# Optimization experiments

Measured on AMD Instinct MI355X. Metric: run time of the kernel, lower is better.

The kernel has to match this reference:

```python
import jax, jax.numpy as jnp
import numpy as np
import math

B, L, D = 4, 4096, 1024
H = 16
DH = D // H  # 64
MAX_SEQ = 8192
NF_MAX = MAX_SEQ // 2 + 1  # 4097
EPS = 1e-6
SQRT2_INV = 1.0 / math.sqrt(2.0)


def _ln(x, scale, bias, eps=1e-5):
    m = jnp.mean(x, axis=-1, keepdims=True)
    v = jnp.mean((x - m) ** 2, axis=-1, keepdims=True)
    return (x - m) * jax.lax.rsqrt(v + eps) * scale + bias


def setup_inputs() -> dict:
    key = jax.random.key(0)
    ks = jax.random.split(key, 16)
    s = 0.02
    inp = {
        'x': jax.random.normal(ks[0], (B, L, D), dtype=jnp.float32),
        'Wq': jax.random.normal(ks[1], (D, D), dtype=jnp.float32) * s,
        'Wv': jax.random.normal(ks[2], (D, D), dtype=jnp.float32) * s,
        'Wo': jax.random.normal(ks[3], (D, D), dtype=jnp.float32) * s,
        # gate MLP: LayerNorm(Dh) -> Linear(Dh,4Dh) -> GELU -> Linear(4Dh, 2*NF_MAX)
        'ln_g_s': jnp.ones((DH,), jnp.float32),
        'ln_g_b': jnp.zeros((DH,), jnp.float32),
        'W1': jax.random.normal(ks[4], (4 * DH, DH), dtype=jnp.float32) * s,
        'b1': jnp.zeros((4 * DH,), jnp.float32),
        'W2': jax.random.normal(ks[5], (2 * NF_MAX, 4 * DH), dtype=jnp.float32) * s,
        'b2': jnp.zeros((2 * NF_MAX,), jnp.float32),
        'modrelu_bias': jnp.zeros((H, NF_MAX), jnp.float32),
        # wavelet gating MLP on head_dim
        'ln_w_s': jnp.ones((DH,), jnp.float32),
        'ln_w_b': jnp.zeros((DH,), jnp.float32),
        'Ww1': jax.random.normal(ks[6], (DH, DH), dtype=jnp.float32) * s,
        'bw1': jnp.zeros((DH,), jnp.float32),
        'Ww2': jax.random.normal(ks[7], (DH, DH), dtype=jnp.float32) * s,
        'bw2': jnp.zeros((DH,), jnp.float32),
    }
    return inp


def _spectre_forward(x, Wq, Wv, Wo, ln_g_s, ln_g_b, W1, b1, W2, b2,
                     modrelu_bias, ln_w_s, ln_w_b, Ww1, bw1, Ww2, bw2):
    b, l, d = x.shape
    n_freq = l // 2 + 1
    # projections -> (B,H,L,Dh)
    q = jnp.einsum('bld,ed->ble', x, Wq).reshape(b, l, H, DH).transpose(0, 2, 1, 3)
    v = jnp.einsum('bld,ed->ble', x, Wv).reshape(b, l, H, DH).transpose(0, 2, 1, 3)
    q_bar = jnp.mean(q, axis=2)  # (B,H,Dh) global query
    # frequency gates from global query
    h = _ln(q_bar, ln_g_s, ln_g_b)
    h = jax.nn.gelu(jnp.einsum('bhd,fd->bhf', h, W1) + b1, approximate=False)
    g = jnp.einsum('bhf,gf->bhg', h, W2) + b2  # (B,H,2*NF_MAX)
    gate = g[..., :n_freq] + 1j * g[..., NF_MAX:NF_MAX + n_freq]  # (B,H,n_freq)
    # spectral mixing along sequence axis
    Vf = jnp.fft.rfft(v, axis=2)  # (B,H,n_freq,Dh) complex
    Vf = Vf * gate[..., None]
    # modReLU nonlinearity on complex spectrum
    mag = jnp.abs(Vf)
    bias = modrelu_bias[None, :, :n_freq, None]
    Vf = Vf * (jax.nn.relu(mag + bias) / (mag + EPS))
    y = jnp.fft.irfft(Vf, n=l, axis=2)  # (B,H,L,Dh)
    # wavelet refinement (eval mode -> never skipped)
    gw = _ln(q_bar, ln_w_s, ln_w_b)
    gw = jax.nn.gelu(jnp.einsum('bhd,ed->bhe', gw, Ww1) + bw1, approximate=False)
    gw = jax.nn.sigmoid(jnp.einsum('bhd,ed->bhe', gw, Ww2) + bw2)  # (B,H,Dh)
    yc = y.transpose(0, 1, 3, 2)  # (B,H,Dh,L)
    low = (yc[..., 0::2] + yc[..., 1::2]) * SQRT2_INV   # Haar analysis LP
    high = (yc[..., 1::2] - yc[..., 0::2]) * SQRT2_INV  # Haar analysis HP
    low = low * gw[..., None]
    high = high * gw[..., None]
    even = (low - high) * SQRT2_INV   # Haar synthesis
    odd = (low + high) * SQRT2_INV
    rec = jnp.stack([even, odd], axis=-1).reshape(b, H, DH, l)  # interleave
    y = y + rec.transpose(0, 1, 3, 2)
    out = jnp.einsum('bld,ed->ble', y.transpose(0, 2, 1, 3).reshape(b, l, d), Wo)
    return out


def reference(x, Wq, Wv, Wo, ln_g_s, ln_g_b, W1, b1, W2, b2,
              modrelu_bias, ln_w_s, ln_w_b, Ww1, bw1, Ww2, bw2):
    return _spectre_forward(x, Wq, Wv, Wo, ln_g_s, ln_g_b, W1, b1, W2, b2,
                            modrelu_bias, ln_w_s, ln_w_b, Ww1, bw1, Ww2, bw2)
```

## Files before the change

### kernel.cpp

```cpp
#include <hip/hip_runtime.h>
#include <math.h>

#define LSEQ 4096
#define DDIM 1024
#define NB 4
#define NH 16
#define DHD 64
#define NFREQ 2049
#define NFMAX 4097

typedef __bf16 bf16_8 __attribute__((ext_vector_type(8)));
typedef float f32x4 __attribute__((ext_vector_type(4)));
typedef float f2 __attribute__((ext_vector_type(2)));

__device__ __forceinline__ float gelu_exact(float v) {
    return 0.5f * v * (1.0f + erff(v * 0.70710678118654752440f));
}

__device__ __forceinline__ void gload16(const void* g, void* l) {
    __builtin_amdgcn_global_load_lds((const __attribute__((address_space(1))) char*)g,
                                     (__attribute__((address_space(3))) char*)l, 16, 0, 0);
}

__global__ __launch_bounds__(256) void k_xbar_partial(const float* __restrict__ x, float* __restrict__ xbp,
                                                      __bf16* __restrict__ xbf) {
    int d = blockIdx.x * 256 + threadIdx.x;
    int chunk = blockIdx.y;
    int b = blockIdx.z;
    size_t base = ((size_t)b * LSEQ + (size_t)chunk * 256) * DDIM + d;
    float acc = 0.f;
    for (int l = 0; l < 256; ++l) {
        float v = x[base + (size_t)l * DDIM];
        acc += v;
        xbf[base + (size_t)l * DDIM] = (__bf16)v;
    }
    xbp[(size_t)(b * 16 + chunk) * DDIM + d] = acc;
}

__global__ __launch_bounds__(256) void k_xbar_reduce(const float* __restrict__ xbp, float* __restrict__ xbar) {
    int d = blockIdx.x * 256 + threadIdx.x;
    int b = blockIdx.y;
    float acc = 0.f;
    for (int c = 0; c < 16; ++c) acc += xbp[(size_t)(b * 16 + c) * DDIM + d];
    xbar[b * DDIM + d] = acc * (1.0f / LSEQ);
}

__global__ __launch_bounds__(256) void k_cvt(const float* __restrict__ s, __bf16* __restrict__ d, int n) {
    int i = (blockIdx.x * 256 + threadIdx.x) * 4;
    if (i < n) {
        float4 v = *(const float4*)(s + i);
        d[i] = (__bf16)v.x; d[i + 1] = (__bf16)v.y; d[i + 2] = (__bf16)v.z; d[i + 3] = (__bf16)v.w;
    }
}

__global__ __launch_bounds__(256) void k_qbar(const float* __restrict__ xbar, const float* __restrict__ Wq,
                                              float* __restrict__ qbar) {
    int lane = threadIdx.x & 63;
    int e = blockIdx.x * 4 + (threadIdx.x >> 6);
    const float* wrow = Wq + (size_t)e * DDIM;
    float a0 = 0, a1 = 0, a2 = 0, a3 = 0;
    for (int i = 0; i < 16; ++i) {
        int d = lane + i * 64;
        float w = wrow[d];
        a0 += w * xbar[d];
        a1 += w * xbar[DDIM + d];
        a2 += w * xbar[2 * DDIM + d];
        a3 += w * xbar[3 * DDIM + d];
    }
    for (int off = 32; off > 0; off >>= 1) {
        a0 += __shfl_down(a0, off);
        a1 += __shfl_down(a1, off);
        a2 += __shfl_down(a2, off);
        a3 += __shfl_down(a3, off);
    }
    if (lane == 0) {
        qbar[e] = a0;
        qbar[DDIM + e] = a1;
        qbar[2 * DDIM + e] = a2;
        qbar[3 * DDIM + e] = a3;
    }
}

__global__ __launch_bounds__(256) void k_mlp(const float* __restrict__ qbar,
                                             const float* __restrict__ ln_g_s, const float* __restrict__ ln_g_b,
                                             const float* __restrict__ W1, const float* __restrict__ b1,
                                             const float* __restrict__ ln_w_s, const float* __restrict__ ln_w_b,
                                             const float* __restrict__ Ww1, const float* __restrict__ bw1,
                                             const float* __restrict__ Ww2, const float* __restrict__ bw2,
                                             float* __restrict__ h1g, float* __restrict__ gwp1) {
    int bh = blockIdx.x;
    __shared__ float q[64], hg[64], hw[64], g1[64];
    __shared__ float sm, sv;
    int t = threadIdx.x;
    if (t < 64) q[t] = qbar[bh * 64 + t];
    __syncthreads();
    if (t == 0) {
        float m = 0;
        for (int i = 0; i < 64; ++i) m += q[i];
        m *= (1.0f / 64.0f);
        float v = 0;
        for (int i = 0; i < 64; ++i) { float dd = q[i] - m; v += dd * dd; }
        v *= (1.0f / 64.0f);
        sm = m; sv = v;
    }
    __syncthreads();
    if (t < 64) {
        float n = (q[t] - sm) * rsqrtf(sv + 1e-5f);
        hg[t] = n * ln_g_s[t] + ln_g_b[t];
        hw[t] = n * ln_w_s[t] + ln_w_b[t];
    }
    __syncthreads();
    {
        int f = t;
        const float* w = W1 + (size_t)f * 64;
        float s = b1[f];
        for (int d0 = 0; d0 < 64; ++d0) s += hg[d0] * w[d0];
        h1g[(size_t)bh * 256 + f] = gelu_exact(s);
    }
    if (t < 64) {
        const float* w = Ww1 + (size_t)t * 64;
        float s = bw1[t];
        for (int k = 0; k < 64; ++k) s += hw[k] * w[k];
        g1[t] = gelu_exact(s);
    }
    __syncthreads();
    if (t < 64) {
        const float* w = Ww2 + (size_t)t * 64;
        float s = bw2[t];
        for (int k = 0; k < 64; ++k) s += g1[k] * w[k];
        gwp1[bh * 64 + t] = 1.0f + 1.0f / (1.0f + expf(-s));
    }
}

__global__ __launch_bounds__(256) void k_gate(const float* __restrict__ h1g, const float* __restrict__ W2,
                                              const float* __restrict__ b2,
                                              float* __restrict__ gre, float* __restrict__ gim) {
    int task = blockIdx.x * 4 + (threadIdx.x >> 6);
    if (task >= 2 * NFREQ) return;
    int lane = threadIdx.x & 63;
    int part = task >= NFREQ;
    int f = task - part * NFREQ;
    int row = part ? (NFMAX + f) : f;
    const float* w = W2 + (size_t)row * 256;
    float w0 = w[lane], w1 = w[64 + lane], w2 = w[128 + lane], w3 = w[192 + lane];
    float bias = b2[row];
    float* dst = part ? gim : gre;
    for (int bh = 0; bh < 64; ++bh) {
        const float* hr = h1g + (size_t)bh * 256;
        float p = w0 * hr[lane] + w1 * hr[64 + lane] + w2 * hr[128 + lane] + w3 * hr[192 + lane];
        for (int off = 32; off > 0; off >>= 1) p += __shfl_down(p, off);
        if (lane == 0) dst[(size_t)bh * NFREQ + f] = p + bias;
    }
}

__device__ __forceinline__ void swz256(int bid, int& n0, int& m0, int& b) {
    int w = (bid & 7) * 32 + (bid >> 3);
    b = w >> 6;
    m0 = ((w >> 2) & 15) << 8;
    n0 = (w & 3) << 8;
}

__device__ __forceinline__ void g4_stage(const __bf16* __restrict__ src, int row0, int kt,
                                         char* buf, int tid) {
#pragma unroll
    for (int j = 0; j < 2; ++j) {
        int c = j * 512 + tid;
        int q = c >> 3, p = c & 7;
        int s3 = p ^ (q & 7);
        int r = 2 * q + (s3 >> 2);
        int kc = (s3 & 3) * 8;
        char* dst = buf + (size_t)(j * 512 + (tid & ~63)) * 16;
        gload16(src + ((size_t)(row0 + r) << 10) + kt * 32 + kc, dst);
    }
}

__device__ __forceinline__ void g4_compute(const char* L, int bi, int wm, int wn,
                                           int lane, f32x4 (&acc)[8][4]) {
    int lrow = lane & 15, lsl = lane >> 4;
    const char* Ab = L + bi * 16384;
    const char* Bb = L + 65536 + bi * 16384;
    int s3 = (lrow & 1) * 4 + lsl;
    bf16_8 af[8], bfr[4];
#pragma unroll
    for (int mi = 0; mi < 8; ++mi) {
        int q = wm * 64 + mi * 8 + (lrow >> 1);
        af[mi] = *(const bf16_8*)(Ab + q * 128 + ((s3 ^ (q & 7)) << 4));
    }
#pragma unroll
    for (int ni = 0; ni < 4; ++ni) {
        int q = wn * 32 + ni * 8 + (lrow >> 1);
        bfr[ni] = *(const bf16_8*)(Bb + q * 128 + ((s3 ^ (q & 7)) << 4));
    }
    __builtin_amdgcn_s_setprio(1);
#pragma unroll
    for (int mi = 0; mi < 8; ++mi)
#pragma unroll
        for (int ni = 0; ni < 4; ++ni)
            acc[mi][ni] = __builtin_amdgcn_mfma_f32_16x16x32_bf16(af[mi], bfr[ni], acc[mi][ni], 0, 0, 0);
    __builtin_amdgcn_s_setprio(0);
}

__device__ __forceinline__ void g4_core(const __bf16* __restrict__ A, const __bf16* __restrict__ B,
                                        int m0, int n0, char* L, f32x4 (&acc)[8][4]) {
    int tid = threadIdx.x;
    int lane = tid & 63, w = tid >> 6;
    int wm = w >> 2, wn = w & 3;
#pragma unroll
    for (int mi = 0; mi < 8; ++mi)
#pragma unroll
        for (int ni = 0; ni < 4; ++ni) acc[mi][ni] = (f32x4){0.f, 0.f, 0.f, 0.f};

#define G4_STAGE(KT, BI)                                   \
    do {                                                   \
        g4_stage(A, m0, (KT), L + (BI) * 16384, tid);      \
        g4_stage(B, n0, (KT), L + 65536 + (BI) * 16384, tid); \
    } while (0)

    G4_STAGE(0, 0);
    G4_STAGE(1, 1);
    G4_STAGE(2, 2);
    asm volatile("s_waitcnt vmcnt(8)" ::: "memory");
    __builtin_amdgcn_s_barrier();
    asm volatile("" ::: "memory");
#pragma unroll 1
    for (int kt = 0; kt < 32; ++kt) {
        int bi = kt & 3;
        if (kt < 29) {
            G4_STAGE(kt + 3, (kt + 3) & 3);
        }
        g4_compute(L, bi, wm, wn, lane, acc);
        asm volatile("s_waitcnt lgkmcnt(0)" ::: "memory");
        if (kt <= 28) {
            asm volatile("s_waitcnt vmcnt(8)" ::: "memory");
        } else if (kt == 29) {
            asm volatile("s_waitcnt vmcnt(4)" ::: "memory");
        } else if (kt == 30) {
            asm volatile("s_waitcnt vmcnt(0)" ::: "memory");
        }
        __builtin_amdgcn_s_barrier();
        asm volatile("" ::: "memory");
    }
#undef G4_STAGE
}

__global__ __launch_bounds__(512, 2) void k_vgemm(const __bf16* __restrict__ xbf, const __bf16* __restrict__ Wvb,
                                                  __bf16* __restrict__ vt) {
    __shared__ __align__(16) char L[131072 + 17408];
    __bf16 (*st)[16][68] = (__bf16(*)[16][68])(L + 131072);
    int n0, m0, b;
    swz256(blockIdx.x, n0, m0, b);
    f32x4 acc[8][4];
    g4_core(xbf + ((size_t)b << 22), Wvb, m0, n0, L, acc);
    int tid = threadIdx.x;
    int lane = tid & 63, w = tid >> 6;
    int wm = w >> 2, wn = w & 3;
    size_t vbase = ((size_t)b << 22);
#pragma unroll
    for (int ni = 0; ni < 4; ++ni) {
#pragma unroll
        for (int half = 0; half < 2; ++half) {
#pragma unroll
            for (int ml = 0; ml < 4; ++ml)
#pragma unroll
                for (int r = 0; r < 4; ++r)
                    st[w][lane & 15][ml * 16 + (lane >> 4) * 4 + r] = (__bf16)acc[half * 4 + ml][ni][r];
            asm volatile("" ::: "memory");
#pragma unroll
            for (int er = 0; er < 16; ++er) {
                vt[vbase + (size_t)(n0 + wn * 64 + ni * 16 + er) * LSEQ + m0 + wm * 128 + half * 64 + lane] =
                    st[w][er][lane];
            }
            asm volatile("" ::: "memory");
        }
    }
}

__global__ __launch_bounds__(512, 2) void k_ogemm(const __bf16* __restrict__ ybf, const __bf16* __restrict__ Wob,
                                                  float* __restrict__ out) {
    __shared__ __align__(16) char L[131072];
    int n0, m0, b;
    swz256(blockIdx.x, n0, m0, b);
    f32x4 acc[8][4];
    g4_core(ybf + ((size_t)b << 22), Wob, m0, n0, L, acc);
    int tid = threadIdx.x;
    int lane = tid & 63, w = tid >> 6;
    int wm = w >> 2, wn = w & 3;
    float* ob = out + ((size_t)b << 22);
#pragma unroll
    for (int mi = 0; mi < 8; ++mi)
#pragma unroll
        for (int ni = 0; ni < 4; ++ni)
#pragma unroll
            for (int r = 0; r < 4; ++r)
                ob[(size_t)(m0 + wm * 128 + mi * 16 + (lane >> 4) * 4 + r) * DDIM +
                   n0 + wn * 64 + ni * 16 + (lane & 15)] = acc[mi][ni][r];
}

__device__ __forceinline__ f2 cmul2(f2 a, f2 b) {
    f2 t = a * (f2){b.x, b.x};
    f2 ayx = __builtin_shufflevector(a, a, 1, 0);
    return t + ayx * (f2){-b.y, b.y};
}
__device__ __forceinline__ f2 mulmi(f2 v) {
    f2 s = __builtin_shufflevector(v, v, 1, 0);
    return s * (f2){1.f, -1.f};
}
__device__ __forceinline__ f2 mulpi(f2 v) {
    f2 s = __builtin_shufflevector(v, v, 1, 0);
    return s * (f2){-1.f, 1.f};
}
__device__ __forceinline__ int P8(int i) { return i + (i >> 3) + (i >> 8); }
__device__ __forceinline__ int SR8(int k) {
    return ((k & 7) << 8) | (((k >> 3) & 7) << 5) | (((k >> 6) & 7) << 2) | (k >> 9);
}

template <int S>
__device__ __forceinline__ void dft4v(f2* x) {
    f2 t0 = x[0] + x[2], t1 = x[0] - x[2];
    f2 t2 = x[1] + x[3], t3 = x[1] - x[3];
    f2 j3 = (S == 1) ? mulmi(t3) : mulpi(t3);
    x[0] = t0 + t2;
    x[2] = t0 - t2;
    x[1] = t1 + j3;
    x[3] = t1 - j3;
}

template <int S>
__device__ __forceinline__ void dft8v(f2* x) {
    f2 e[4] = {x[0], x[2], x[4], x[6]};
    f2 o[4] = {x[1], x[3], x[5], x[7]};
    dft4v<S>(e);
    dft4v<S>(o);
    const float c = 0.7071067811865476f;
    const float sg = (S == 1) ? -1.f : 1.f;
    o[1] = cmul2(o[1], (f2){c, sg * c});
    o[2] = (S == 1) ? mulmi(o[2]) : mulpi(o[2]);
    o[3] = cmul2(o[3], (f2){-c, sg * c});
    x[0] = e[0] + o[0];
    x[4] = e[0] - o[0];
    x[1] = e[1] + o[1];
    x[5] = e[1] - o[1];
    x[2] = e[2] + o[2];
    x[6] = e[2] - o[2];
    x[3] = e[3] + o[3];
    x[7] = e[3] - o[3];
}

template <int S>
__device__ __forceinline__ void tw8(f2* x, int j, float invN) {
    float base = ((S == 1) ? -6.283185307179586f : 6.283185307179586f) * invN;
    float sn, cs;
    __sincosf(base * (float)j, &sn, &cs);
    f2 w1 = (f2){cs, sn};
    f2 w2 = cmul2(w1, w1);
    f2 w3 = cmul2(w2, w1);
    f2 w4 = cmul2(w2, w2);
    f2 w5 = cmul2(w4, w1);
    f2 w6 = cmul2(w4, w2);
    f2 w7 = cmul2(w4, w3);
    x[1] = cmul2(x[1], w1);
    x[2] = cmul2(x[2], w2);
    x[3] = cmul2(x[3], w3);
    x[4] = cmul2(x[4], w4);
    x[5] = cmul2(x[5], w5);
    x[6] = cmul2(x[6], w6);
    x[7] = cmul2(x[7], w7);
}

__global__ __launch_bounds__(256, 2) void k_fft(__bf16* __restrict__ vty,
                                                const float* __restrict__ gre, const float* __restrict__ gim,
                                                const float* __restrict__ mrb, const float* __restrict__ gwp1) {
    __shared__ f2 Zp[2312];
    int pid = blockIdx.x;
    int b = pid >> 10, e = pid & 1023;
    int h = e >> 6, dh = e & 63;
    int bh = b * 16 + h;
    size_t gbase = (size_t)bh * NFREQ;
    size_t mbase = (size_t)h * NFMAX;
    __bf16* row = vty + ((size_t)b << 22) + ((size_t)e << 12);
    int t = threadIdx.x;

#pragma unroll
    for (int cc = 0; cc < 2; ++cc) {
        int c = t + cc * 256;
        bf16_8 a = *(const bf16_8*)&row[c * 8];
#pragma unroll
        for (int q = 0; q < 4; ++q)
            Zp[P8(c * 4 + q)] = (f2){(float)a[2 * q], (float)a[2 * q + 1]};
    }
    __syncthreads();

    f2 x[8];
    {
#pragma unroll
        for (int r = 0; r < 8; ++r) x[r] = Zp[P8(r * 256 + t)];
        dft8v<1>(x);
        tw8<1>(x, t, 1.0f / 2048.0f);
#pragma unroll
        for (int r = 0; r < 8; ++r) Zp[P8(r * 256 + t)] = x[r];
    }
    __syncthreads();
    {
        int g = t >> 5, j = t & 31, base = g * 256 + j;
#pragma unroll
        for (int r = 0; r < 8; ++r) x[r] = Zp[P8(base + r * 32)];
        dft8v<1>(x);
        tw8<1>(x, j, 1.0f / 256.0f);
#pragma unroll
        for (int r = 0; r < 8; ++r) Zp[P8(base + r * 32)] = x[r];
    }
    __syncthreads();
    {
        int g = t >> 2, j = t & 3, base = g * 32 + j;
#pragma unroll
        for (int r = 0; r < 8; ++r) x[r] = Zp[P8(base + r * 4)];
        dft8v<1>(x);
        tw8<1>(x, j, 1.0f / 32.0f);
#pragma unroll
        for (int r = 0; r < 8; ++r) Zp[P8(base + r * 4)] = x[r];
    }
    __syncthreads();
    {
        int base = t * 8;
#pragma unroll
        for (int q = 0; q < 4; ++q) { x[q] = Zp[P8(base + q)]; x[4 + q] = Zp[P8(base + 4 + q)]; }
        dft4v<1>(x);
        dft4v<1>(x + 4);
#pragma unroll
        for (int q = 0; q < 4; ++q) { Zp[P8(base + q)] = x[q]; Zp[P8(base + 4 + q)] = x[4 + q]; }
    }
    __syncthreads();

    {
        float sn0, cs0;
        __sincosf(-1.5339807878856412e-3f * (float)(1 + t), &sn0, &cs0);
        f2 wk = (f2){cs0, sn0};
        const f2 W256 = (f2){0.92387953251128675613f, -0.38268343236508977172f};
#pragma unroll
        for (int r = 0; r < 4; ++r) {
            int k = 1 + (r << 8) + t;
            int k2 = 2048 - k;
            int sA = P8(SR8(k)), sB = P8(SR8(k2));
            float cs = wk.x, sn = wk.y;
            f2 Za = Zp[sA], Zb = Zp[sB];
            float Er = 0.5f * (Za.x + Zb.x), Ei = 0.5f * (Za.y - Zb.y);
            float Dr = 0.5f * (Za.x - Zb.x), Di = 0.5f * (Za.y + Zb.y);
            float WDr = cs * Dr - sn * Di, WDi = cs * Di + sn * Dr;
            float Tr = -WDi, Ti = WDr;
            float Vkr = Er - Tr, Vki = Ei - Ti;
            float Vk2r = Er + Tr, Vk2i = -(Ei + Ti);
            float g1r = gre[gbase + k], g1i = gim[gbase + k], b1v = mrb[mbase + k];
            float Ykr = Vkr * g1r - Vki * g1i, Yki = Vkr * g1i + Vki * g1r;
            float m1 = sqrtf(Ykr * Ykr + Yki * Yki);
            float s1 = fmaxf(m1 + b1v, 0.f) / (m1 + 1e-6f);
            Ykr *= s1; Yki *= s1;
            float g2r = gre[gbase + k2], g2i = gim[gbase + k2], b2v = mrb[mbase + k2];
            float Yk2r = Vk2r * g2r - Vk2i * g2i, Yk2i = Vk2r * g2i + Vk2i * g2r;
            float m2 = sqrtf(Yk2r * Yk2r + Yk2i * Yk2i);
            float s2 = fmaxf(m2 + b2v, 0.f) / (m2 + 1e-6f);
            Yk2r *= s2; Yk2i *= s2;
            float Epr = 0.5f * (Ykr + Yk2r), Epi = 0.5f * (Yki - Yk2i);
            float Fr = 0.5f * (Ykr - Yk2r), Fi = 0.5f * (Yki + Yk2i);
            float CWFr = cs * Fr + sn * Fi;
            float CWFi = cs * Fi - sn * Fr;
            Zp[sA] = (f2){Epr - CWFi, Epi + CWFr};
            Zp[sB] = (f2){Epr + CWFi, -Epi + CWFr};
            wk = cmul2(wk, W256);
        }
    }
    if (t == 0) {
        f2 Z0 = Zp[P8(0)];
        float V0 = Z0.x + Z0.y, VN = Z0.x - Z0.y;
        float g0r = gre[gbase], g0i = gim[gbase], b0v = mrb[mbase];
        float y0r = V0 * g0r, y0i = V0 * g0i;
        float m0 = sqrtf(y0r * y0r + y0i * y0i);
        float Y0 = y0r * (fmaxf(m0 + b0v, 0.f) / (m0 + 1e-6f));
        float gNr = gre[gbase + 2048], gNi = gim[gbase + 2048], bNv = mrb[mbase + 2048];
        float yNr = VN * gNr, yNi = VN * gNi;
        float mN = sqrtf(yNr * yNr + yNi * yNi);
        float YN = yNr * (fmaxf(mN + bNv, 0.f) / (mN + 1e-6f));
        Zp[P8(0)] = (f2){0.5f * (Y0 + YN), 0.5f * (Y0 - YN)};
    }
    __syncthreads();

    {
        int base = t * 8;
#pragma unroll
        for (int q = 0; q < 4; ++q) { x[q] = Zp[P8(base + q)]; x[4 + q] = Zp[P8(base + 4 + q)]; }
        dft4v<-1>(x);
        dft4v<-1>(x + 4);
#pragma unroll
        for (int q = 0; q < 4; ++q) { Zp[P8(base + q)] = x[q]; Zp[P8(base + 4 + q)] = x[4 + q]; }
    }
    __syncthreads();
    {
        int g = t >> 2, j = t & 3, base = g * 32 + j;
#pragma unroll
        for (int r = 0; r < 8; ++r) x[r] = Zp[P8(base + r * 4)];
        tw8<-1>(x, j, 1.0f / 32.0f);
        dft8v<-1>(x);
#pragma unroll
        for (int r = 0; r < 8; ++r) Zp[P8(base + r * 4)] = x[r];
    }
    __syncthreads();
    {
        int g = t >> 5, j = t & 31, base = g * 256 + j;
#pragma unroll
        for (int r = 0; r < 8; ++r) x[r] = Zp[P8(base + r * 32)];
        tw8<-1>(x, j, 1.0f / 256.0f);
        dft8v<-1>(x);
#pragma unroll
        for (int r = 0; r < 8; ++r) Zp[P8(base + r * 32)] = x[r];
    }
    __syncthreads();
    {
#pragma unroll
        for (int r = 0; r < 8; ++r) x[r] = Zp[P8(r * 256 + t)];
        tw8<-1>(x, t, 1.0f / 2048.0f);
        dft8v<-1>(x);
        float sc = gwp1[bh * 64 + dh] * (1.0f / 2048.0f);
        unsigned int* row32 = (unsigned int*)row;
#pragma unroll
        for (int r = 0; r < 8; ++r) {
            __bf16 h1 = (__bf16)(x[r].x * sc);
            __bf16 h2 = (__bf16)(x[r].y * sc);
            unsigned int u = (unsigned int)__builtin_bit_cast(unsigned short, h1) |
                             ((unsigned int)__builtin_bit_cast(unsigned short, h2) << 16);
            row32[t + 256 * r] = u;
        }
    }
}

__global__ __launch_bounds__(256) void k_t2(const __bf16* __restrict__ vt, __bf16* __restrict__ ybf) {
    __shared__ __bf16 tl[64][66];
    int e0 = blockIdx.x * 64, l0 = blockIdx.y * 64, b = blockIdx.z;
    int t = threadIdx.x;
    const __bf16* src = vt + ((size_t)b << 22);
    __bf16* dst = ybf + ((size_t)b << 22);
    int er = t >> 3, lc = (t & 7) * 8;
#pragma unroll
    for (int it = 0; it < 2; ++it) {
        int e = er + it * 32;
        bf16_8 v = *(const bf16_8*)&src[(size_t)(e0 + e) * LSEQ + l0 + lc];
#pragma unroll
        for (int j = 0; j < 8; ++j) tl[e][lc + j] = v[j];
    }
    __syncthreads();
    int lr = t >> 3, ec = (t & 7) * 8;
#pragma unroll
    for (int it = 0; it < 2; ++it) {
        int l = lr + it * 32;
        bf16_8 v;
#pragma unroll
        for (int j = 0; j < 8; ++j) v[j] = tl[ec + j][l];
        *(bf16_8*)&dst[(size_t)(l0 + l) * DDIM + e0 + ec] = v;
    }
}

extern "C" void kernel_launch(void* const* d_in, const int* in_sizes, int n_in,
                              void* d_out, int out_size, void* d_ws, size_t ws_size,
                              hipStream_t stream) {
    const float* x      = (const float*)d_in[0];
    const float* Wq     = (const float*)d_in[1];
    const float* Wv     = (const float*)d_in[2];
    const float* Wo     = (const float*)d_in[3];
    const float* ln_g_s = (const float*)d_in[4];
    const float* ln_g_b = (const float*)d_in[5];
    const float* W1     = (const float*)d_in[6];
    const float* b1     = (const float*)d_in[7];
    const float* W2     = (const float*)d_in[8];
    const float* b2     = (const float*)d_in[9];
    const float* mrb    = (const float*)d_in[10];
    const float* ln_w_s = (const float*)d_in[11];
    const float* ln_w_b = (const float*)d_in[12];
    const float* Ww1    = (const float*)d_in[13];
    const float* bw1    = (const float*)d_in[14];
    const float* Ww2    = (const float*)d_in[15];
    const float* bw2    = (const float*)d_in[16];
    float* out = (float*)d_out;

    char* W = (char*)d_ws;
    __bf16* xbf = (__bf16*)W;
    __bf16* ybf = xbf;
    __bf16* Wvb = (__bf16*)(W + 33554432);
    __bf16* Wob = (__bf16*)(W + 35651584);
    float*  xbp = (float*)(W + 37748736);
    float*  xbar= (float*)(W + 38010880);
    float*  qbar= (float*)(W + 38027264);
    float*  h1g = (float*)(W + 38043648);
    float*  gwp1= (float*)(W + 38109184);
    float*  gre = (float*)(W + 38125568);
    float*  gim = (float*)(W + 38650112);

    __bf16* vt = (__bf16*)d_out;

    k_xbar_partial<<<dim3(4, 16, 4), 256, 0, stream>>>(x, xbp, xbf);
    k_cvt<<<1024, 256, 0, stream>>>(Wv, Wvb, DDIM * DDIM);
    k_cvt<<<1024, 256, 0, stream>>>(Wo, Wob, DDIM * DDIM);
    k_xbar_reduce<<<dim3(4, 4), 256, 0, stream>>>(xbp, xbar);
    k_qbar<<<256, 256, 0, stream>>>(xbar, Wq, qbar);
    k_mlp<<<64, 256, 0, stream>>>(qbar, ln_g_s, ln_g_b, W1, b1, ln_w_s, ln_w_b,
                                  Ww1, bw1, Ww2, bw2, h1g, gwp1);
    k_gate<<<1025, 256, 0, stream>>>(h1g, W2, b2, gre, gim);
    k_vgemm<<<256, 512, 0, stream>>>(xbf, Wvb, vt);
    k_fft<<<4096, 256, 0, stream>>>(vt, gre, gim, mrb, gwp1);
    k_t2<<<dim3(16, 64, 4), 256, 0, stream>>>(vt, ybf);
    k_ogemm<<<256, 512, 0, stream>>>(ybf, Wob, out);
}
```

Before: 194.3 us.

## Shrink GEMM tiles to 128x256 with 3-stage LDS ring for more blocks

The V-projection and output-projection GEMMs now use 128x256 tiles instead of 256x256, which doubles the grid to 512 blocks. The shared-memory ring drops from 4 stages to 3 and LDS use falls from about 144KB to 72KB. Launch bounds rise to allow 4 blocks per CU, and the block swizzle is updated for the new tile count. The aim is to fill all CUs on the MI355X and gain occupancy, at the cost of lower arithmetic intensity per tile, more redundant loads of the B operand, and a shallower prefetch pipeline.

```diff
diff --git a/kernel.cpp b/kernel.cpp
--- a/kernel.cpp
+++ b/kernel.cpp
@@ -153,17 +153,18 @@
     }
 }
 
-__device__ __forceinline__ void swz256(int bid, int& n0, int& m0, int& b) {
-    int w = (bid & 7) * 32 + (bid >> 3);
-    b = w >> 6;
-    m0 = ((w >> 2) & 15) << 8;
+__device__ __forceinline__ void swz512(int bid, int& n0, int& m0, int& b) {
+    int w = (bid & 7) * 64 + (bid >> 3);
+    b = w >> 7;
+    m0 = ((w >> 2) & 31) << 7;
     n0 = (w & 3) << 8;
 }
 
-__device__ __forceinline__ void g4_stage(const __bf16* __restrict__ src, int row0, int kt,
+template <int NCH>
+__device__ __forceinline__ void g5_stage(const __bf16* __restrict__ src, int row0, int kt,
                                          char* buf, int tid) {
 #pragma unroll
-    for (int j = 0; j < 2; ++j) {
+    for (int j = 0; j < NCH; ++j) {
         int c = j * 512 + tid;
         int q = c >> 3, p = c & 7;
         int s3 = p ^ (q & 7);
@@ -174,16 +175,16 @@
     }
 }
 
-__device__ __forceinline__ void g4_compute(const char* L, int bi, int wm, int wn,
-                                           int lane, f32x4 (&acc)[8][4]) {
+__device__ __forceinline__ void g5_compute(const char* L, int bi, int wm, int wn,
+                                           int lane, f32x4 (&acc)[4][4]) {
     int lrow = lane & 15, lsl = lane >> 4;
-    const char* Ab = L + bi * 16384;
-    const char* Bb = L + 65536 + bi * 16384;
+    const char* Ab = L + bi * 8192;
+    const char* Bb = L + 24576 + bi * 16384;
     int s3 = (lrow & 1) * 4 + lsl;
-    bf16_8 af[8], bfr[4];
-#pragma unroll
-    for (int mi = 0; mi < 8; ++mi) {
-        int q = wm * 64 + mi * 8 + (lrow >> 1);
+    bf16_8 af[4], bfr[4];
+#pragma unroll
+    for (int mi = 0; mi < 4; ++mi) {
+        int q = wm * 32 + mi * 8 + (lrow >> 1);
         af[mi] = *(const bf16_8*)(Ab + q * 128 + ((s3 ^ (q & 7)) << 4));
     }
 #pragma unroll
@@ -193,64 +194,60 @@
     }
     __builtin_amdgcn_s_setprio(1);
 #pragma unroll
-    for (int mi = 0; mi < 8; ++mi)
+    for (int mi = 0; mi < 4; ++mi)
 #pragma unroll
         for (int ni = 0; ni < 4; ++ni)
             acc[mi][ni] = __builtin_amdgcn_mfma_f32_16x16x32_bf16(af[mi], bfr[ni], acc[mi][ni], 0, 0, 0);
     __builtin_amdgcn_s_setprio(0);
 }
 
-__device__ __forceinline__ void g4_core(const __bf16* __restrict__ A, const __bf16* __restrict__ B,
-                                        int m0, int n0, char* L, f32x4 (&acc)[8][4]) {
+__device__ __forceinline__ void g5_core(const __bf16* __restrict__ A, const __bf16* __restrict__ B,
+                                        int m0, int n0, char* L, f32x4 (&acc)[4][4]) {
     int tid = threadIdx.x;
     int lane = tid & 63, w = tid >> 6;
     int wm = w >> 2, wn = w & 3;
 #pragma unroll
-    for (int mi = 0; mi < 8; ++mi)
+    for (int mi = 0; mi < 4; ++mi)
 #pragma unroll
         for (int ni = 0; ni < 4; ++ni) acc[mi][ni] = (f32x4){0.f, 0.f, 0.f, 0.f};
 
-#define G4_STAGE(KT, BI)                                   \
-    do {                                                   \
-        g4_stage(A, m0, (KT), L + (BI) * 16384, tid);      \
-        g4_stage(B, n0, (KT), L + 65536 + (BI) * 16384, tid); \
+#define G5_STAGE(KT, BI)                                        \
+    do {                                                        \
+        g5_stage<1>(A, m0, (KT), L + (BI) * 8192, tid);         \
+        g5_stage<2>(B, n0, (KT), L + 24576 + (BI) * 16384, tid);\
     } while (0)
 
-    G4_STAGE(0, 0);
-    G4_STAGE(1, 1);
-    G4_STAGE(2, 2);
-    asm volatile("s_waitcnt vmcnt(8)" ::: "memory");
+    G5_STAGE(0, 0);
+    G5_STAGE(1, 1);
+    asm volatile("s_waitcnt vmcnt(3)" ::: "memory");
     __builtin_amdgcn_s_barrier();
     asm volatile("" ::: "memory");
 #pragma unroll 1
     for (int kt = 0; kt < 32; ++kt) {
-        int bi = kt & 3;
-        if (kt < 29) {
-            G4_STAGE(kt + 3, (kt + 3) & 3);
+        if (kt < 30) {
+            G5_STAGE(kt + 2, (kt + 2) % 3);
         }
-        g4_compute(L, bi, wm, wn, lane, acc);
+        g5_compute(L, kt % 3, wm, wn, lane, acc);
         asm volatile("s_waitcnt lgkmcnt(0)" ::: "memory");
-        if (kt <= 28) {
-            asm volatile("s_waitcnt vmcnt(8)" ::: "memory");
-        } else if (kt == 29) {
-            asm volatile("s_waitcnt vmcnt(4)" ::: "memory");
+        if (kt < 30) {
+            asm volatile("s_waitcnt vmcnt(3)" ::: "memory");
         } else if (kt == 30) {
             asm volatile("s_waitcnt vmcnt(0)" ::: "memory");
         }
         __builtin_amdgcn_s_barrier();
         asm volatile("" ::: "memory");
     }
-#undef G4_STAGE
-}
-
-__global__ __launch_bounds__(512, 2) void k_vgemm(const __bf16* __restrict__ xbf, const __bf16* __restrict__ Wvb,
+#undef G5_STAGE
+}
+
+__global__ __launch_bounds__(512, 4) void k_vgemm(const __bf16* __restrict__ xbf, const __bf16* __restrict__ Wvb,
                                                   __bf16* __restrict__ vt) {
-    __shared__ __align__(16) char L[131072 + 17408];
-    __bf16 (*st)[16][68] = (__bf16(*)[16][68])(L + 131072);
+    __shared__ __align__(16) char L[73728];
     int n0, m0, b;
-    swz256(blockIdx.x, n0, m0, b);
-    f32x4 acc[8][4];
-    g4_core(xbf + ((size_t)b << 22), Wvb, m0, n0, L, acc);
+    swz512(blockIdx.x, n0, m0, b);
+    f32x4 acc[4][4];
+    g5_core(xbf + ((size_t)b << 22), Wvb, m0, n0, L, acc);
+    __bf16 (*st)[16][68] = (__bf16(*)[16][68])L;
     int tid = threadIdx.x;
     int lane = tid & 63, w = tid >> 6;
     int wm = w >> 2, wn = w & 3;
@@ -258,41 +255,38 @@
 #pragma unroll
     for (int ni = 0; ni < 4; ++ni) {
 #pragma unroll
-        for (int half = 0; half < 2; ++half) {
-#pragma unroll
-            for (int ml = 0; ml < 4; ++ml)
-#pragma unroll
-                for (int r = 0; r < 4; ++r)
-                    st[w][lane & 15][ml * 16 + (lane >> 4) * 4 + r] = (__bf16)acc[half * 4 + ml][ni][r];
-            asm volatile("" ::: "memory");
-#pragma unroll
-            for (int er = 0; er < 16; ++er) {
-                vt[vbase + (size_t)(n0 + wn * 64 + ni * 16 + er) * LSEQ + m0 + wm * 128 + half * 64 + lane] =
-                    st[w][er][lane];
-            }
-            asm volatile("" ::: "memory");
+        for (int ml = 0; ml < 4; ++ml)
+#pragma unroll
+            for (int r = 0; r < 4; ++r)
+                st[w][lane & 15][ml * 16 + (lane >> 4) * 4 + r] = (__bf16)acc[ml][ni][r];
+        asm volatile("" ::: "memory");
+#pragma unroll
+        for (int er = 0; er < 16; ++er) {
+            vt[vbase + (size_t)(n0 + wn * 64 + ni * 16 + er) * LSEQ + m0 + wm * 64 + lane] =
+                st[w][er][lane];
         }
-    }
-}
-
-__global__ __launch_bounds__(512, 2) void k_ogemm(const __bf16* __restrict__ ybf, const __bf16* __restrict__ Wob,
+        asm volatile("" ::: "memory");
+    }
+}
+
+__global__ __launch_bounds__(512, 4) void k_ogemm(const __bf16* __restrict__ ybf, const __bf16* __restrict__ Wob,
                                                   float* __restrict__ out) {
-    __shared__ __align__(16) char L[131072];
+    __shared__ __align__(16) char L[73728];
     int n0, m0, b;
-    swz256(blockIdx.x, n0, m0, b);
-    f32x4 acc[8][4];
-    g4_core(ybf + ((size_t)b << 22), Wob, m0, n0, L, acc);
+    swz512(blockIdx.x, n0, m0, b);
+    f32x4 acc[4][4];
+    g5_core(ybf + ((size_t)b << 22), Wob, m0, n0, L, acc);
     int tid = threadIdx.x;
     int lane = tid & 63, w = tid >> 6;
     int wm = w >> 2, wn = w & 3;
     float* ob = out + ((size_t)b << 22);
 #pragma unroll
-    for (int mi = 0; mi < 8; ++mi)
+    for (int mi = 0; mi < 4; ++mi)
 #pragma unroll
         for (int ni = 0; ni < 4; ++ni)
 #pragma unroll
             for (int r = 0; r < 4; ++r)
-                ob[(size_t)(m0 + wm * 128 + mi * 16 + (lane >> 4) * 4 + r) * DDIM +
+                ob[(size_t)(m0 + wm * 64 + mi * 16 + (lane >> 4) * 4 + r) * DDIM +
                    n0 + wn * 64 + ni * 16 + (lane & 15)] = acc[mi][ni][r];
 }
 
@@ -602,8 +596,8 @@
     k_mlp<<<64, 256, 0, stream>>>(qbar, ln_g_s, ln_g_b, W1, b1, ln_w_s, ln_w_b,
                                   Ww1, bw1, Ww2, bw2, h1g, gwp1);
     k_gate<<<1025, 256, 0, stream>>>(h1g, W2, b2, gre, gim);
-    k_vgemm<<<256, 512, 0, stream>>>(xbf, Wvb, vt);
+    k_vgemm<<<512, 512, 0, stream>>>(xbf, Wvb, vt);
     k_fft<<<4096, 256, 0, stream>>>(vt, gre, gim, mrb, gwp1);
     k_t2<<<dim3(16, 64, 4), 256, 0, stream>>>(vt, ybf);
-    k_ogemm<<<256, 512, 0, stream>>>(ybf, Wob, out);
-}
+    k_ogemm<<<512, 512, 0, stream>>>(ybf, Wob, out);
+}
```

Measured after the change: 197.6 us. Within noise of the previous version (+1.7%).

## Restructure bf16 GEMM mainloop into double-buffered 64-wide K stages with interleaved loads

Applied to the files above, without the earlier changes.

Replaces the 4-slot, 32-wide K pipeline in the shared V- and output-projection GEMM core with a 2-slot, 64-wide K double buffer. Each iteration is split into four phases that interleave LDS fragment reads, MFMA batches and async global-to-LDS loads for the next stage. The aim is to hide LDS reads behind MFMA work and overlap global loads with compute, so the core runs at higher MFMA throughput. In exchange it adds many more barriers per iteration and a shallower prefetch depth, which could expose global-load latency.

```diff
diff --git a/kernel.cpp b/kernel.cpp
--- a/kernel.cpp
+++ b/kernel.cpp
@@ -160,7 +160,7 @@
     n0 = (w & 3) << 8;
 }
 
-__device__ __forceinline__ void g4_stage(const __bf16* __restrict__ src, int row0, int kt,
+__device__ __forceinline__ void g6_stage(const __bf16* __restrict__ src, int row0, int kcol0,
                                          char* buf, int tid) {
 #pragma unroll
     for (int j = 0; j < 2; ++j) {
@@ -170,77 +170,106 @@
         int r = 2 * q + (s3 >> 2);
         int kc = (s3 & 3) * 8;
         char* dst = buf + (size_t)(j * 512 + (tid & ~63)) * 16;
-        gload16(src + ((size_t)(row0 + r) << 10) + kt * 32 + kc, dst);
-    }
-}
-
-__device__ __forceinline__ void g4_compute(const char* L, int bi, int wm, int wn,
-                                           int lane, f32x4 (&acc)[8][4]) {
-    int lrow = lane & 15, lsl = lane >> 4;
-    const char* Ab = L + bi * 16384;
-    const char* Bb = L + 65536 + bi * 16384;
-    int s3 = (lrow & 1) * 4 + lsl;
-    bf16_8 af[8], bfr[4];
-#pragma unroll
-    for (int mi = 0; mi < 8; ++mi) {
-        int q = wm * 64 + mi * 8 + (lrow >> 1);
-        af[mi] = *(const bf16_8*)(Ab + q * 128 + ((s3 ^ (q & 7)) << 4));
-    }
-#pragma unroll
-    for (int ni = 0; ni < 4; ++ni) {
-        int q = wn * 32 + ni * 8 + (lrow >> 1);
-        bfr[ni] = *(const bf16_8*)(Bb + q * 128 + ((s3 ^ (q & 7)) << 4));
-    }
+        gload16(src + ((size_t)(row0 + r) << 10) + kcol0 + kc, dst);
+    }
+}
+
+__device__ __forceinline__ void g6_readA(const char* Ah, int wm, int lrow, int lsl, int mi0, bf16_8* af) {
+#pragma unroll
+    for (int i = 0; i < 4; ++i) {
+        int r = wm * 128 + (mi0 + i) * 16 + lrow;
+        int q = r >> 1;
+        int s3 = (r & 1) * 4 + lsl;
+        af[i] = *(const bf16_8*)(Ah + q * 128 + ((s3 ^ (q & 7)) << 4));
+    }
+}
+
+__device__ __forceinline__ void g6_readB(const char* Bh, int wn, int lrow, int lsl, bf16_8* bfr) {
+#pragma unroll
+    for (int i = 0; i < 4; ++i) {
+        int r = wn * 64 + i * 16 + lrow;
+        int q = r >> 1;
+        int s3 = (r & 1) * 4 + lsl;
+        bfr[i] = *(const bf16_8*)(Bh + q * 128 + ((s3 ^ (q & 7)) << 4));
+    }
+}
+
+__device__ __forceinline__ void g6_mfma16(const bf16_8* af, const bf16_8* bfr, int mi0, f32x4 (&acc)[8][4]) {
     __builtin_amdgcn_s_setprio(1);
 #pragma unroll
-    for (int mi = 0; mi < 8; ++mi)
-#pragma unroll
-        for (int ni = 0; ni < 4; ++ni)
-            acc[mi][ni] = __builtin_amdgcn_mfma_f32_16x16x32_bf16(af[mi], bfr[ni], acc[mi][ni], 0, 0, 0);
+    for (int i = 0; i < 4; ++i)
+#pragma unroll
+        for (int j = 0; j < 4; ++j)
+            acc[mi0 + i][j] = __builtin_amdgcn_mfma_f32_16x16x32_bf16(af[i], bfr[j], acc[mi0 + i][j], 0, 0, 0);
     __builtin_amdgcn_s_setprio(0);
 }
 
-__device__ __forceinline__ void g4_core(const __bf16* __restrict__ A, const __bf16* __restrict__ B,
+#define BAR()  do { __builtin_amdgcn_s_barrier(); asm volatile("" ::: "memory"); } while (0)
+#define LGKM0() asm volatile("s_waitcnt lgkmcnt(0)" ::: "memory")
+#define VM(n)   asm volatile("s_waitcnt vmcnt(" #n ")" ::: "memory")
+
+__device__ __forceinline__ void g6_core(const __bf16* __restrict__ A, const __bf16* __restrict__ B,
                                         int m0, int n0, char* L, f32x4 (&acc)[8][4]) {
     int tid = threadIdx.x;
     int lane = tid & 63, w = tid >> 6;
     int wm = w >> 2, wn = w & 3;
+    int lrow = lane & 15, lsl = lane >> 4;
 #pragma unroll
     for (int mi = 0; mi < 8; ++mi)
 #pragma unroll
         for (int ni = 0; ni < 4; ++ni) acc[mi][ni] = (f32x4){0.f, 0.f, 0.f, 0.f};
 
-#define G4_STAGE(KT, BI)                                   \
-    do {                                                   \
-        g4_stage(A, m0, (KT), L + (BI) * 16384, tid);      \
-        g4_stage(B, n0, (KT), L + 65536 + (BI) * 16384, tid); \
-    } while (0)
-
-    G4_STAGE(0, 0);
-    G4_STAGE(1, 1);
-    G4_STAGE(2, 2);
-    asm volatile("s_waitcnt vmcnt(8)" ::: "memory");
-    __builtin_amdgcn_s_barrier();
-    asm volatile("" ::: "memory");
+#define AS(s, h) (L + (s) * 32768 + (h) * 16384)
+#define BS(s, h) (L + 65536 + (s) * 32768 + (h) * 16384)
+
+    g6_stage(A, m0, 0, AS(0, 0), tid);
+    g6_stage(B, n0, 0, BS(0, 0), tid);
+    g6_stage(A, m0, 32, AS(0, 1), tid);
+    g6_stage(B, n0, 32, BS(0, 1), tid);
+    VM(4);
+    BAR();
+
 #pragma unroll 1
-    for (int kt = 0; kt < 32; ++kt) {
-        int bi = kt & 3;
-        if (kt < 29) {
-            G4_STAGE(kt + 3, (kt + 3) & 3);
-        }
-        g4_compute(L, bi, wm, wn, lane, acc);
-        asm volatile("s_waitcnt lgkmcnt(0)" ::: "memory");
-        if (kt <= 28) {
-            asm volatile("s_waitcnt vmcnt(8)" ::: "memory");
-        } else if (kt == 29) {
-            asm volatile("s_waitcnt vmcnt(4)" ::: "memory");
-        } else if (kt == 30) {
-            asm volatile("s_waitcnt vmcnt(0)" ::: "memory");
-        }
-        __builtin_amdgcn_s_barrier();
-        asm volatile("" ::: "memory");
-    }
-#undef G4_STAGE
+    for (int kt = 0; kt < 16; ++kt) {
+        int s = kt & 1, sn = s ^ 1;
+        const char* A0 = AS(s, 0);
+        const char* A1 = AS(s, 1);
+        const char* B0 = BS(s, 0);
+        const char* B1 = BS(s, 1);
+        bf16_8 af[4], bfr[4];
+        int kn = (kt + 1) * 64;
+
+        g6_readB(B0, wn, lrow, lsl, bfr);
+        g6_readA(A0, wm, lrow, lsl, 0, af);
+        if (kt < 15) g6_stage(A, m0, kn, AS(sn, 0), tid);
+        BAR();
+        LGKM0();
+        g6_mfma16(af, bfr, 0, acc);
+        BAR();
+        g6_readA(A0, wm, lrow, lsl, 4, af);
+        if (kt < 15) g6_stage(B, n0, kn, BS(sn, 0), tid);
+        BAR();
+        LGKM0();
+        g6_mfma16(af, bfr, 4, acc);
+        if (kt < 15) { VM(4); } else { VM(0); }
+        BAR();
+        g6_readB(B1, wn, lrow, lsl, bfr);
+        g6_readA(A1, wm, lrow, lsl, 0, af);
+        if (kt < 15) g6_stage(A, m0, kn + 32, AS(sn, 1), tid);
+        BAR();
+        LGKM0();
+        g6_mfma16(af, bfr, 0, acc);
+        BAR();
+        g6_readA(A1, wm, lrow, lsl, 4, af);
+        if (kt < 15) g6_stage(B, n0, kn + 32, BS(sn, 1), tid);
+        BAR();
+        LGKM0();
+        g6_mfma16(af, bfr, 4, acc);
+        if (kt < 15) { VM(4); }
+        BAR();
+    }
+#undef AS
+#undef BS
 }
 
 __global__ __launch_bounds__(512, 2) void k_vgemm(const __bf16* __restrict__ xbf, const __bf16* __restrict__ Wvb,
@@ -250,7 +279,7 @@
     int n0, m0, b;
     swz256(blockIdx.x, n0, m0, b);
     f32x4 acc[8][4];
-    g4_core(xbf + ((size_t)b << 22), Wvb, m0, n0, L, acc);
+    g6_core(xbf + ((size_t)b << 22), Wvb, m0, n0, L, acc);
     int tid = threadIdx.x;
     int lane = tid & 63, w = tid >> 6;
     int wm = w >> 2, wn = w & 3;
@@ -281,7 +310,7 @@
     int n0, m0, b;
     swz256(blockIdx.x, n0, m0, b);
     f32x4 acc[8][4];
-    g4_core(ybf + ((size_t)b << 22), Wob, m0, n0, L, acc);
+    g6_core(ybf + ((size_t)b << 22), Wob, m0, n0, L, acc);
     int tid = threadIdx.x;
     int lane = tid & 63, w = tid >> 6;
     int wm = w >> 2, wn = w & 3;
```

After: 194.9 us. Within noise of the previous version (+0.3%).
